# Optimization experiments

Measured on AMD Instinct MI355X. Metric: run time of the kernel, lower is better.

## Reference

```python
import jax, jax.numpy as jnp
import numpy as np
import math

B = 2
LAYERS = 18
LATENT = 512
MAPPER_LAYER = 7  # w_code_num[attention_layer=11]
CLUSTERS = 10
CLUSTER_LAYER = 11
CLUSTER_DIM = 512 + 2 * (512 // 16)  # 576
LR_MUL = 0.1
LAYER_NUM = [0, 2, 3, 5, 6, 8, 9, 11, 12, 14, 15, 17, 18, 20, 21, 23, 24]
CH = [512] * 11 + [256] * 2 + [128] * 3 + [64] * 3 + [32] * 3 + [16] * 3
RES = [4, 8, 8, 16, 16, 32, 32, 64, 64, 128, 128] + [256] * 14


def _forward(x, fmaps, mw, mb, afw, afb, aw, ab, alw, alb, initial_state):
    batch = x.shape[0]
    blend = fmaps[CLUSTER_LAYER - 1]
    size = blend.shape[2]  # 128

    # ---- cluster assignment (torch.no_grad block) ----
    pc = blend.shape[1] // 16  # position_channel = 32
    coords = jnp.arange(size, dtype=jnp.float32) * (2.0 / (size - 1)) - 1.0
    xp = jnp.broadcast_to(coords[None, :], (size, size))
    yp = jnp.broadcast_to(coords[:, None], (size, size))
    cf = jnp.concatenate([
        blend,
        jnp.broadcast_to(xp[None, None], (batch, pc, size, size)),
        jnp.broadcast_to(yp[None, None], (batch, pc, size, size)),
    ], axis=1)
    cf = jax.lax.stop_gradient(cf)
    flat = cf.transpose(0, 2, 3, 1).reshape(-1, cf.shape[1])  # [B*S*S, 576]
    dis = (jnp.sum(flat * flat, axis=1, keepdims=True)
           - 2.0 * flat @ initial_state.T
           + jnp.sum(initial_state * initial_state, axis=1)[None, :])
    assign = jnp.argmin(dis, axis=1).reshape(batch, size, size)
    choice = jnp.arange(batch)[:, None, None] * CLUSTERS + assign  # [B,S,S]

    x7 = x[:, :MAPPER_LAYER, -LATENT:]
    h = x7 * jax.lax.rsqrt(jnp.mean(x7 * x7, axis=-1, keepdims=True) + 1e-8)
    w_scale = (1.0 / math.sqrt(LATENT)) * LR_MUL
    for i in range(3):
        h = jnp.einsum('bci,coi->bco', h, mw[:, i]) * w_scale
        h = jax.nn.leaky_relu(h + mb[:, i][None] * LR_MUL, 0.2) * math.sqrt(2.0)
    delta_zs = jnp.concatenate(
        [h, jnp.zeros((batch, LAYERS - MAPPER_LAYER, LATENT), h.dtype)], axis=1)
    loss_delta = jnp.mean(jnp.sqrt(jnp.sum(delta_zs[:, :MAPPER_LAYER] ** 2, axis=-1)))

    # ---- attention branch (EqualConv2d 1x1 + nearest interpolate, torch semantics) ----
    def conv1x1(f, w, b):
        cin = f.shape[1]
        return jnp.einsum('bihw,oi->bohw', f, w) * (1.0 / math.sqrt(cin)) + b[None, :, None, None]

    def interp(f):  # torch nearest: src = floor(i * in / out)
        H = f.shape[2]
        idx = (jnp.arange(size) * H) // size
        return f[:, :, idx][:, :, :, idx]

    att = [interp(conv1x1(fmaps[-1], afw, afb))]
    for c in range(LAYERS - 1):
        f = fmaps[LAYER_NUM[c]]
        att.append(interp(conv1x1(f, aw[c][:, :f.shape[1]], ab[c])))
    amap = jnp.concatenate(att, axis=1)  # [B, 32*18, S, S]
    logits = jnp.einsum('bihw,i->bhw', amap, alw) * (1.0 / math.sqrt(32 * LAYERS)) + alb[0]
    each = jax.nn.sigmoid(logits)  # [B,S,S]

    # ---- training branch: per-(batch,cluster) masked mean -> segment mean ----
    nseg = batch * CLUSTERS
    seg = choice.reshape(-1)
    vals = each.reshape(-1)
    sums = jax.ops.segment_sum(vals, seg, num_segments=nseg)
    cnts = jax.ops.segment_sum(jnp.ones_like(vals), seg, num_segments=nseg)
    mean = sums / jnp.maximum(cnts, 1.0)
    attention_map = jnp.where(cnts > 0, mean, 1.0)[choice]  # [B,S,S]
    loss_reg = jnp.sum(jnp.where(cnts > 0, jnp.maximum(mean - 0.8, 0.0), 0.0)) / batch
    loss_tv = jnp.mean((each - jax.lax.stop_gradient(attention_map)) ** 2)

    am = attention_map[:, None]  # [B,1,S,S]
    final = jnp.where(am < 0.8, am - jax.lax.stop_gradient(am), am)
    # torchvision gaussian_blur(k=5): sigma = 0.3*((5-1)*0.5-1)+0.8 = 1.1, reflect pad
    xs = jnp.linspace(-2.0, 2.0, 5)
    k1 = jnp.exp(-0.5 * (xs / 1.1) ** 2)
    k1 = k1 / jnp.sum(k1)
    k2 = jnp.outer(k1, k1)[None, None]  # [1,1,5,5]
    padded = jnp.pad(final, ((0, 0), (0, 0), (2, 2), (2, 2)), mode='reflect')
    blurred = jax.lax.conv_general_dilated(padded, k2.astype(final.dtype), (1, 1), 'VALID')
    return delta_zs, blurred, loss_delta, loss_reg, loss_tv


def setup_inputs() -> dict:
    key = jax.random.key(0)
    ks = jax.random.split(key, 40)
    inp = {}
    inp['x'] = jax.random.normal(ks[0], (B, LAYERS, LATENT), jnp.float32)
    for i in range(25):
        inp[f'fmap_{i}'] = jax.random.normal(ks[1 + i], (B, CH[i], RES[i], RES[i]), jnp.float32)
    inp['fmap_25'] = jax.random.normal(ks[26], (B, 512, 4, 4), jnp.float32)
    inp['mw'] = jax.random.normal(ks[27], (MAPPER_LAYER, 3, LATENT, LATENT), jnp.float32)
    inp['mb'] = 0.1 * jax.random.normal(ks[28], (MAPPER_LAYER, 3, LATENT), jnp.float32)
    inp['afw'] = jax.random.normal(ks[29], (32, 512), jnp.float32)
    inp['afb'] = 0.1 * jax.random.normal(ks[30], (32,), jnp.float32)
    inp['aw'] = jax.random.normal(ks[31], (LAYERS - 1, 32, 512), jnp.float32)
    inp['ab'] = 0.1 * jax.random.normal(ks[32], (LAYERS - 1, 32), jnp.float32)
    inp['alw'] = jax.random.normal(ks[33], (32 * LAYERS,), jnp.float32)
    inp['alb'] = jnp.full((1,), 5.0, jnp.float32)  # attention_last bias init to 5
    inp['initial_state'] = jax.random.normal(ks[34], (CLUSTERS, CLUSTER_DIM), jnp.float32)
    inp['size'] = 128
    return inp


def reference(x, fmap_0, fmap_1, fmap_2, fmap_3, fmap_4, fmap_5, fmap_6, fmap_7,
              fmap_8, fmap_9, fmap_10, fmap_11, fmap_12, fmap_13, fmap_14, fmap_15,
              fmap_16, fmap_17, fmap_18, fmap_19, fmap_20, fmap_21, fmap_22, fmap_23,
              fmap_24, fmap_25, mw, mb, afw, afb, aw, ab, alw, alb, initial_state, size):
    fmaps = [fmap_0, fmap_1, fmap_2, fmap_3, fmap_4, fmap_5, fmap_6, fmap_7, fmap_8,
             fmap_9, fmap_10, fmap_11, fmap_12, fmap_13, fmap_14, fmap_15, fmap_16,
             fmap_17, fmap_18, fmap_19, fmap_20, fmap_21, fmap_22, fmap_23, fmap_24,
             fmap_25]
    return _forward(x, fmaps, mw, mb, afw, afb, aw, ab, alw, alb, initial_state)
```

## Files before the change

### kernel.cpp

```cpp
#include <hip/hip_runtime.h>
#include <math.h>

#define NPIX 32768
#define OUT_DZ 0
#define OUT_BLUR 18432
#define OUT_LD 51200
#define OUT_REG 51201
#define OUT_TV 51202
#define NSLAB 30

__constant__ int d_cin[18] = {512,512,512,512,512,512,512,512,256,256,128,128,64,64,32,32,16,16};
__constant__ int d_H[18]   = {4,  4,  8,  16, 32, 32, 64, 128,256,256,256,256,256,256,256,256,256,256};

__constant__ int d_slab_t[NSLAB]  = {0,1,2,3,4,5, 6,6, 7,7,7,7, 8,8,8,8, 9,9,9,9, 10,10, 11,11, 12,13,14,15,16,17};
__constant__ int d_slab_c0[NSLAB] = {0,0,0,0,0,0, 0,256, 0,128,256,384, 0,64,128,192, 0,64,128,192, 0,64, 0,64, 0,0,0,0,0,0};
__constant__ int d_slab_nc[NSLAB] = {512,512,512,512,512,512, 256,256, 128,128,128,128, 64,64,64,64, 64,64,64,64, 64,64, 64,64, 64,64,32,32,16,16};

struct FPtrs { const float* f[18]; };

#define WS_HA     0
#define WS_HB     7168
#define WS_ST     14336
#define WS_CN     22528
#define WS_BIASP  22576
#define WS_V      22656
#define WS_CHOICE 31872
#define WS_PART   64640
#define WS_EACH   1047680
#define WS_SUMS   1080448
#define WS_CNTS   1083008
#define WS_ATTV   1085568
#define WS_TVP    1085600

__global__ __launch_bounds__(512) void k_vfold(
    const float* __restrict__ afw, const float* __restrict__ afb,
    const float* __restrict__ aw,  const float* __restrict__ ab,
    const float* __restrict__ alw, const float* __restrict__ istate,
    float* __restrict__ v, float* __restrict__ biasp,
    float* __restrict__ st, float* __restrict__ cn)
{
    int t = blockIdx.x;
    if (t < 18) {
        int cin = d_cin[t];
        const float* w  = (t==0) ? afw : aw + (size_t)(t-1)*32*512;
        const float* bb = (t==0) ? afb : ab + (t-1)*32;
        float scale = (1.0f/sqrtf((float)cin)) * (1.0f/24.0f);
        int c = threadIdx.x;
        if (c < cin) {
            float s = 0.0f;
            #pragma unroll 8
            for (int o = 0; o < 32; o++) s += alw[t*32+o] * w[o*512 + c];
            v[t*512 + c] = s * scale;
        }
        if (threadIdx.x == 0) {
            float s = 0.0f;
            for (int o = 0; o < 32; o++) s += alw[t*32+o] * bb[o];
            biasp[t] = s * (1.0f/24.0f);
        }
    } else {
        int c = threadIdx.x;
        if (c < 512) {
            #pragma unroll
            for (int j = 0; j < 10; j++) st[c*16 + j] = -2.0f * istate[j*576 + c];
        }
        if (c < 10) {
            int j = c;
            float n = 0.0f, s1 = 0.0f, s2 = 0.0f;
            for (int k = 0; k < 576; k++) { float sv = istate[j*576+k]; n += sv*sv; }
            for (int k = 512; k < 544; k++) s1 += istate[j*576+k];
            for (int k = 544; k < 576; k++) s2 += istate[j*576+k];
            cn[j] = n; cn[16+j] = -2.0f*s1; cn[32+j] = -2.0f*s2;
        }
    }
}

__global__ __launch_bounds__(256) void k_assign(
    const float* __restrict__ blend, const float* __restrict__ st,
    const float* __restrict__ cn, int* __restrict__ choice)
{
    __shared__ float gsh[256*10];
    int tid = threadIdx.x;
    int csub = __builtin_amdgcn_readfirstlane(tid >> 6);
    int pl = tid & 63;
    int p = blockIdx.x*64 + pl;
    int b = p >> 14, rem = p & 16383;
    float g[10] = {0,0,0,0,0,0,0,0,0,0};
    const float* src = blend + ((size_t)b*512 + csub*128)*16384 + rem;
    const float* stc = st + csub*128*16;
    for (int c0 = 0; c0 < 128; c0 += 8) {
        float q[8];
        #pragma unroll
        for (int u = 0; u < 8; u++) q[u] = src[(size_t)(c0+u) << 14];
        #pragma unroll
        for (int u = 0; u < 8; u++) {
            #pragma unroll
            for (int j = 0; j < 10; j++) g[j] = fmaf(q[u], stc[(c0+u)*16 + j], g[j]);
        }
    }
    #pragma unroll
    for (int j = 0; j < 10; j++) gsh[tid*10 + j] = g[j];
    __syncthreads();
    if (tid < 64) {
        int pp = blockIdx.x*64 + tid;
        int bb = pp >> 14, rr = pp & 16383, y = rr >> 7, x = rr & 127;
        float cx = (float)x * (float)(2.0/127.0) - 1.0f;
        float cy = (float)y * (float)(2.0/127.0) - 1.0f;
        float gt[10];
        #pragma unroll
        for (int j = 0; j < 10; j++) {
            gt[j] = cn[j] + cn[16+j]*cx + cn[32+j]*cy
                  + gsh[tid*10 + j] + gsh[(64+tid)*10 + j]
                  + gsh[(128+tid)*10 + j] + gsh[(192+tid)*10 + j];
        }
        int best = 0; float bg = gt[0];
        #pragma unroll
        for (int j = 1; j < 10; j++) if (gt[j] < bg) { bg = gt[j]; best = j; }
        choice[pp] = bb*10 + best;
    }
}

__global__ __launch_bounds__(256) void k_norm(const float* __restrict__ x, float* __restrict__ h)
{
    int r = blockIdx.x;
    int b = r / 7, c = r % 7;
    const float* xr = x + ((size_t)b*18 + c)*512;
    int tid = threadIdx.x;
    float v0 = xr[tid], v1 = xr[tid+256];
    __shared__ float red[256];
    __shared__ float scale;
    red[tid] = v0*v0 + v1*v1; __syncthreads();
    for (int s = 128; s; s >>= 1) { if (tid < s) red[tid] += red[tid+s]; __syncthreads(); }
    if (tid == 0) scale = 1.0f / sqrtf(red[0]*(1.0f/512.0f) + 1e-8f);
    __syncthreads();
    h[r*512 + tid] = v0*scale; h[r*512 + 256 + tid] = v1*scale;
}

__global__ __launch_bounds__(256) void k_mlp(
    const float* __restrict__ mw, const float* __restrict__ mb,
    const float* __restrict__ hin, float* __restrict__ hout,
    int layer, float* __restrict__ dz)
{
    int wave = blockIdx.x*4 + (threadIdx.x >> 6);
    int lane = threadIdx.x & 63;
    int c = wave >> 9, o = wave & 511;
    const float* wrow = mw + (((size_t)(c*3 + layer)*512 + o) << 9) + lane*8;
    float4 w0 = *(const float4*)wrow;
    float4 w1 = *(const float4*)(wrow + 4);
    const float* h0 = hin + (size_t)c*512 + lane*8;
    const float* h1 = hin + (size_t)(7 + c)*512 + lane*8;
    float4 a0 = *(const float4*)h0, a1 = *(const float4*)(h0+4);
    float4 b0 = *(const float4*)h1, b1 = *(const float4*)(h1+4);
    float d0 = a0.x*w0.x + a0.y*w0.y + a0.z*w0.z + a0.w*w0.w
             + a1.x*w1.x + a1.y*w1.y + a1.z*w1.z + a1.w*w1.w;
    float d1 = b0.x*w0.x + b0.y*w0.y + b0.z*w0.z + b0.w*w0.w
             + b1.x*w1.x + b1.y*w1.y + b1.z*w1.z + b1.w*w1.w;
    #pragma unroll
    for (int m = 32; m; m >>= 1) { d0 += __shfl_xor(d0, m); d1 += __shfl_xor(d1, m); }
    if (lane == 0) {
        const float wsc = (float)(0.1/22.62741699796952);
        const float rt2 = 1.41421356237309515f;
        float bias = mb[(c*3 + layer)*512 + o] * 0.1f;
        float z0 = d0*wsc + bias; z0 = (z0 > 0.0f ? z0 : 0.2f*z0) * rt2;
        float z1 = d1*wsc + bias; z1 = (z1 > 0.0f ? z1 : 0.2f*z1) * rt2;
        hout[(size_t)c*512 + o] = z0;
        hout[(size_t)(7 + c)*512 + o] = z1;
        if (dz) {
            dz[((size_t)0*18 + c)*512 + o] = z0;
            dz[((size_t)1*18 + c)*512 + o] = z1;
        }
    }
}

__global__ __launch_bounds__(256) void k_lossdelta(const float* __restrict__ h, float* __restrict__ outp)
{
    __shared__ float red[256];
    int tid = threadIdx.x;
    float total = 0.0f;
    for (int r = 0; r < 14; r++) {
        float v0 = h[r*512 + tid], v1 = h[r*512 + 256 + tid];
        red[tid] = v0*v0 + v1*v1; __syncthreads();
        for (int s = 128; s; s >>= 1) { if (tid < s) red[tid] += red[tid+s]; __syncthreads(); }
        if (tid == 0) total += sqrtf(red[0]);
        __syncthreads();
    }
    if (tid == 0) outp[0] = total * (1.0f/14.0f);
}

__global__ __launch_bounds__(256) void k_zero(float* __restrict__ out)
{
    int z = blockIdx.x*256 + threadIdx.x;
    if (z < 11264) {
        int b = z / (11*512), rem = z % (11*512);
        out[(size_t)b*18*512 + 7*512 + rem] = 0.0f;
    }
}

__global__ __launch_bounds__(256) void k_each(FPtrs fp, const float* __restrict__ v, float* __restrict__ partial)
{
    __shared__ float vsh[512];
    int s  = blockIdx.x >> 6;
    int px = blockIdx.x & 63;
    int t  = d_slab_t[s];
    int c0 = d_slab_c0[s];
    int nc = d_slab_nc[s];
    int H  = d_H[t];
    int cin = d_cin[t];
    int tid  = threadIdx.x;
    for (int i = tid; i < nc; i += 256) vsh[i] = v[t*512 + c0 + i];
    __syncthreads();
    int row  = tid >> 6;
    int lane = tid & 63;
    int pbase = px*512;
    int b = pbase >> 14;
    int y = ((pbase & 16383) >> 7) + row;
    const float* base = fp.f[t] + (size_t)(b*cin + c0) * (size_t)(H*H);
    float a0 = 0.0f, a1 = 0.0f;

    if (H == 256) {
        const float* src = base + (size_t)(2*y)*256 + 4*lane;
        for (int cc = 0; cc < nc; cc += 8) {
            float4 q[8];
            #pragma unroll
            for (int u = 0; u < 8; u++) q[u] = *(const float4*)(src + (size_t)(cc+u)*65536);
            #pragma unroll
            for (int u = 0; u < 8; u++) {
                float vv = vsh[cc+u];
                a0 = fmaf(q[u].x, vv, a0); a1 = fmaf(q[u].z, vv, a1);
            }
        }
    } else if (H == 128) {
        const float* src = base + (size_t)y*128 + 2*lane;
        for (int cc = 0; cc < nc; cc += 8) {
            float2 q[8];
            #pragma unroll
            for (int u = 0; u < 8; u++) q[u] = *(const float2*)(src + (size_t)(cc+u)*16384);
            #pragma unroll
            for (int u = 0; u < 8; u++) {
                float vv = vsh[cc+u];
                a0 = fmaf(q[u].x, vv, a0); a1 = fmaf(q[u].y, vv, a1);
            }
        }
    } else if (H == 64) {
        const float* src = base + (size_t)(y >> 1)*64 + lane;
        for (int cc = 0; cc < nc; cc += 8) {
            float q[8];
            #pragma unroll
            for (int u = 0; u < 8; u++) q[u] = src[(size_t)(cc+u)*4096];
            #pragma unroll
            for (int u = 0; u < 8; u++) {
                float vv = vsh[cc+u];
                a0 = fmaf(q[u], vv, a0); a1 = fmaf(q[u], vv, a1);
            }
        }
    } else {
        int x0 = 2*lane, x1 = 2*lane + 1;
        int sy = (y*H) >> 7, sx0 = (x0*H) >> 7, sx1 = (x1*H) >> 7;
        const float* src = base + (size_t)sy*H;
        size_t HH = (size_t)H*H;
        for (int cc = 0; cc < nc; cc += 8) {
            float q0[8], q1[8];
            #pragma unroll
            for (int u = 0; u < 8; u++) {
                q0[u] = src[(size_t)(cc+u)*HH + sx0];
                q1[u] = src[(size_t)(cc+u)*HH + sx1];
            }
            #pragma unroll
            for (int u = 0; u < 8; u++) {
                float vv = vsh[cc+u];
                a0 = fmaf(q0[u], vv, a0); a1 = fmaf(q1[u], vv, a1);
            }
        }
    }
    int p = pbase + row*128 + 2*lane;
    float2 o; o.x = a0; o.y = a1;
    *(float2*)(partial + (size_t)s*NPIX + p) = o;
}

__global__ __launch_bounds__(256) void k_logits(
    const float* __restrict__ partial, const float* __restrict__ biasp,
    const float* __restrict__ alb, const int* __restrict__ choice,
    float* __restrict__ each, float* __restrict__ bsums, int* __restrict__ bcnts)
{
    __shared__ float ssum[20]; __shared__ int scnt[20]; __shared__ float sbias;
    int tid = threadIdx.x;
    if (tid < 20) { ssum[tid] = 0.0f; scnt[tid] = 0; }
    if (tid == 0) {
        float s = alb[0];
        for (int t = 0; t < 18; t++) s += biasp[t];
        sbias = s;
    }
    __syncthreads();
    int p = blockIdx.x*256 + tid;
    float lg = sbias;
    #pragma unroll
    for (int s = 0; s < NSLAB; s++) lg += partial[(size_t)s*NPIX + p];
    float e = 1.0f / (1.0f + expf(-lg));
    each[p] = e;
    int ch = choice[p];
    atomicAdd(&ssum[ch], e);
    atomicAdd(&scnt[ch], 1);
    __syncthreads();
    if (tid < 20) { bsums[blockIdx.x*20 + tid] = ssum[tid]; bcnts[blockIdx.x*20 + tid] = scnt[tid]; }
}

__global__ __launch_bounds__(64) void k_stats(
    const float* __restrict__ bsums, const int* __restrict__ bcnts,
    float* __restrict__ attv, float* __restrict__ out)
{
    __shared__ float red[32];
    int j = threadIdx.x;
    float regj = 0.0f;
    if (j < 20) {
        float s = 0.0f; int c = 0;
        for (int blk = 0; blk < 128; blk++) { s += bsums[blk*20 + j]; c += bcnts[blk*20 + j]; }
        float mean = s / fmaxf((float)c, 1.0f);
        attv[j] = (c > 0) ? mean : 1.0f;
        regj = (c > 0) ? fmaxf(mean - 0.8f, 0.0f) : 0.0f;
    }
    if (j < 32) red[j] = (j < 20) ? regj : 0.0f;
    __syncthreads();
    for (int s = 16; s; s >>= 1) { if (j < s) red[j] += red[j+s]; __syncthreads(); }
    if (j == 0) out[OUT_REG] = red[0] * 0.5f;
}

__global__ __launch_bounds__(256) void k_final(
    const float* __restrict__ each, const int* __restrict__ choice,
    const float* __restrict__ attv, float* __restrict__ tvp, float* __restrict__ out)
{
    __shared__ float av[20];
    __shared__ float red[256];
    int tid = threadIdx.x;
    if (tid < 20) av[tid] = attv[tid];
    __syncthreads();
    int p = blockIdx.x*256 + tid;
    int b = p >> 14, rem = p & 16383, y = rem >> 7, x = rem & 127;
    float k1[5]; float ks = 0.0f;
    #pragma unroll
    for (int i = 0; i < 5; i++) { float d = (float)(i-2) / 1.1f; k1[i] = expf(-0.5f*d*d); ks += k1[i]; }
    #pragma unroll
    for (int i = 0; i < 5; i++) k1[i] /= ks;
    const int* cb = choice + b*16384;
    float acc = 0.0f;
    #pragma unroll
    for (int a = 0; a < 5; a++) {
        int yy = y + a - 2; yy = (yy < 0) ? -yy : ((yy > 127) ? 254 - yy : yy);
        #pragma unroll
        for (int bb = 0; bb < 5; bb++) {
            int xx = x + bb - 2; xx = (xx < 0) ? -xx : ((xx > 127) ? 254 - xx : xx);
            float am = av[cb[yy*128 + xx]];
            float fin = (am < 0.8f) ? 0.0f : am;
            acc += k1[a]*k1[bb]*fin;
        }
    }
    out[OUT_BLUR + p] = acc;
    float amc = av[cb[y*128 + x]];
    float d = each[p] - amc;
    red[tid] = d*d; __syncthreads();
    for (int s = 128; s; s >>= 1) { if (tid < s) red[tid] += red[tid+s]; __syncthreads(); }
    if (tid == 0) tvp[blockIdx.x] = red[0];
}

__global__ __launch_bounds__(128) void k_tvred(const float* __restrict__ tvp, float* __restrict__ out)
{
    __shared__ float red[128];
    int tid = threadIdx.x;
    red[tid] = tvp[tid]; __syncthreads();
    for (int s = 64; s; s >>= 1) { if (tid < s) red[tid] += red[tid+s]; __syncthreads(); }
    if (tid == 0) out[OUT_TV] = red[0] * (1.0f/32768.0f);
}

extern "C" void kernel_launch(void* const* d_in, const int* in_sizes, int n_in,
                              void* d_out, int out_size, void* d_ws, size_t ws_size,
                              hipStream_t stream)
{
    const float* x      = (const float*)d_in[0];
    const float* blend  = (const float*)d_in[11];
    const float* mw     = (const float*)d_in[27];
    const float* mb     = (const float*)d_in[28];
    const float* afw    = (const float*)d_in[29];
    const float* afb    = (const float*)d_in[30];
    const float* aw     = (const float*)d_in[31];
    const float* ab     = (const float*)d_in[32];
    const float* alw    = (const float*)d_in[33];
    const float* alb    = (const float*)d_in[34];
    const float* istate = (const float*)d_in[35];
    float* out = (float*)d_out;
    float* ws  = (float*)d_ws;

    static const int LN[17] = {0,2,3,5,6,8,9,11,12,14,15,17,18,20,21,23,24};
    FPtrs fp;
    fp.f[0] = (const float*)d_in[26];
    for (int c = 0; c < 17; c++) fp.f[1+c] = (const float*)d_in[1 + LN[c]];

    float* hA     = ws + WS_HA;
    float* hB     = ws + WS_HB;
    float* st     = ws + WS_ST;
    float* cn     = ws + WS_CN;
    float* biasp  = ws + WS_BIASP;
    float* v      = ws + WS_V;
    int*   choice = (int*)(ws + WS_CHOICE);
    float* part   = ws + WS_PART;
    float* each   = ws + WS_EACH;
    float* bsums  = ws + WS_SUMS;
    int*   bcnts  = (int*)(ws + WS_CNTS);
    float* attv   = ws + WS_ATTV;
    float* tvp    = ws + WS_TVP;

    k_vfold<<<dim3(19), 512, 0, stream>>>(afw, afb, aw, ab, alw, istate, v, biasp, st, cn);
    k_norm<<<14, 256, 0, stream>>>(x, hA);
    k_mlp<<<896, 256, 0, stream>>>(mw, mb, hA, hB, 0, nullptr);
    k_mlp<<<896, 256, 0, stream>>>(mw, mb, hB, hA, 1, nullptr);
    k_mlp<<<896, 256, 0, stream>>>(mw, mb, hA, hB, 2, out + OUT_DZ);
    k_lossdelta<<<1, 256, 0, stream>>>(hB, out + OUT_LD);
    k_zero<<<44, 256, 0, stream>>>(out);
    k_assign<<<512, 256, 0, stream>>>(blend, st, cn, choice);
    k_each<<<NSLAB*64, 256, 0, stream>>>(fp, v, part);
    k_logits<<<128, 256, 0, stream>>>(part, biasp, alb, choice, each, bsums, bcnts);
    k_stats<<<1, 64, 0, stream>>>(bsums, bcnts, attv, out);
    k_final<<<128, 256, 0, stream>>>(each, choice, attv, tvp, out);
    k_tvred<<<1, 128, 0, stream>>>(tvp, out);
}
```

Measured before the change: 159.7 us.

## Retile attention partial sums and cluster assignment for more pixels per thread

Splits the large-resolution feature maps into finer channel slabs (48 instead of 30) and gives those slabs a new block mapping where each wave handles four rows with wider float4 loads. Cluster assignment now uses 512-thread blocks where each thread covers two pixels and each of eight waves sums 64 channels. The aim is more memory-level parallelism and better occupancy on the bandwidth-bound feature-map reads. In exchange, more partial-sum slabs must be written and reduced in the logits kernel, and the workspace offsets grow to fit them.

After: 163.5 us. 1.02x slower.

```diff
diff --git a/kernel.cpp b/kernel.cpp
--- a/kernel.cpp
+++ b/kernel.cpp
@@ -7,14 +7,29 @@
 #define OUT_LD 51200
 #define OUT_REG 51201
 #define OUT_TV 51202
-#define NSLAB 30
+#define NSLAB 48
 
 __constant__ int d_cin[18] = {512,512,512,512,512,512,512,512,256,256,128,128,64,64,32,32,16,16};
 __constant__ int d_H[18]   = {4,  4,  8,  16, 32, 32, 64, 128,256,256,256,256,256,256,256,256,256,256};
 
-__constant__ int d_slab_t[NSLAB]  = {0,1,2,3,4,5, 6,6, 7,7,7,7, 8,8,8,8, 9,9,9,9, 10,10, 11,11, 12,13,14,15,16,17};
-__constant__ int d_slab_c0[NSLAB] = {0,0,0,0,0,0, 0,256, 0,128,256,384, 0,64,128,192, 0,64,128,192, 0,64, 0,64, 0,0,0,0,0,0};
-__constant__ int d_slab_nc[NSLAB] = {512,512,512,512,512,512, 256,256, 128,128,128,128, 64,64,64,64, 64,64,64,64, 64,64, 64,64, 64,64,32,32,16,16};
+__constant__ int d_slab_t[NSLAB]  = {0,1,2,3,4,5, 6,6,
+                                     7,7,7,7,7,7,7,7,
+                                     8,8,8,8,8,8,8,8,
+                                     9,9,9,9,9,9,9,9,
+                                     10,10,10,10, 11,11,11,11,
+                                     12,12, 13,13, 14, 15, 16, 17};
+__constant__ int d_slab_c0[NSLAB] = {0,0,0,0,0,0, 0,256,
+                                     0,64,128,192,256,320,384,448,
+                                     0,32,64,96,128,160,192,224,
+                                     0,32,64,96,128,160,192,224,
+                                     0,32,64,96, 0,32,64,96,
+                                     0,32, 0,32, 0, 0, 0, 0};
+__constant__ int d_slab_nc[NSLAB] = {512,512,512,512,512,512, 256,256,
+                                     64,64,64,64,64,64,64,64,
+                                     32,32,32,32,32,32,32,32,
+                                     32,32,32,32,32,32,32,32,
+                                     32,32,32,32, 32,32,32,32,
+                                     32,32, 32,32, 32, 32, 16, 16};
 
 struct FPtrs { const float* f[18]; };
 
@@ -26,11 +41,11 @@
 #define WS_V      22656
 #define WS_CHOICE 31872
 #define WS_PART   64640
-#define WS_EACH   1047680
-#define WS_SUMS   1080448
-#define WS_CNTS   1083008
-#define WS_ATTV   1085568
-#define WS_TVP    1085600
+#define WS_EACH   1637504
+#define WS_SUMS   1670272
+#define WS_CNTS   1672832
+#define WS_ATTV   1675392
+#define WS_TVP    1675424
 
 __global__ __launch_bounds__(512) void k_vfold(
     const float* __restrict__ afw, const float* __restrict__ afb,
@@ -74,48 +89,57 @@
     }
 }
 
-__global__ __launch_bounds__(256) void k_assign(
+__global__ __launch_bounds__(512, 4) void k_assign(
     const float* __restrict__ blend, const float* __restrict__ st,
     const float* __restrict__ cn, int* __restrict__ choice)
 {
-    __shared__ float gsh[256*10];
-    int tid = threadIdx.x;
-    int csub = __builtin_amdgcn_readfirstlane(tid >> 6);
-    int pl = tid & 63;
-    int p = blockIdx.x*64 + pl;
-    int b = p >> 14, rem = p & 16383;
-    float g[10] = {0,0,0,0,0,0,0,0,0,0};
-    const float* src = blend + ((size_t)b*512 + csub*128)*16384 + rem;
-    const float* stc = st + csub*128*16;
-    for (int c0 = 0; c0 < 128; c0 += 8) {
-        float q[8];
+    __shared__ float gsh[8*128*10];
+    int tid = threadIdx.x;
+    int w = tid >> 6, lane = tid & 63;
+    int csub = __builtin_amdgcn_readfirstlane(w);
+    int pw = blockIdx.x * 128;
+    int b = pw >> 14, rem = pw & 16383;
+    const float* src = blend + ((size_t)b*512 + csub*64)*16384 + rem + 2*lane;
+    const float* stc = st + csub*64*16;
+    float g0[10] = {0,0,0,0,0,0,0,0,0,0};
+    float g1[10] = {0,0,0,0,0,0,0,0,0,0};
+    for (int c0 = 0; c0 < 64; c0 += 4) {
+        float2 q[4];
         #pragma unroll
-        for (int u = 0; u < 8; u++) q[u] = src[(size_t)(c0+u) << 14];
+        for (int u = 0; u < 4; u++) q[u] = *(const float2*)(src + (size_t)(c0+u)*16384);
         #pragma unroll
-        for (int u = 0; u < 8; u++) {
-            #pragma unroll
-            for (int j = 0; j < 10; j++) g[j] = fmaf(q[u], stc[(c0+u)*16 + j], g[j]);
+        for (int u = 0; u < 4; u++) {
+            #pragma unroll
+            for (int j = 0; j < 10; j++) {
+                float sv = stc[(c0+u)*16 + j];
+                g0[j] = fmaf(q[u].x, sv, g0[j]);
+                g1[j] = fmaf(q[u].y, sv, g1[j]);
+            }
         }
     }
     #pragma unroll
-    for (int j = 0; j < 10; j++) gsh[tid*10 + j] = g[j];
-    __syncthreads();
-    if (tid < 64) {
-        int pp = blockIdx.x*64 + tid;
-        int bb = pp >> 14, rr = pp & 16383, y = rr >> 7, x = rr & 127;
+    for (int j = 0; j < 10; j++) {
+        gsh[(w*128 + 2*lane)*10 + j]     = g0[j];
+        gsh[(w*128 + 2*lane + 1)*10 + j] = g1[j];
+    }
+    __syncthreads();
+    if (tid < 128) {
+        int p = pw + tid;
+        int bb = p >> 14, rr = p & 16383, y = rr >> 7, x = rr & 127;
         float cx = (float)x * (float)(2.0/127.0) - 1.0f;
         float cy = (float)y * (float)(2.0/127.0) - 1.0f;
         float gt[10];
         #pragma unroll
         for (int j = 0; j < 10; j++) {
-            gt[j] = cn[j] + cn[16+j]*cx + cn[32+j]*cy
-                  + gsh[tid*10 + j] + gsh[(64+tid)*10 + j]
-                  + gsh[(128+tid)*10 + j] + gsh[(192+tid)*10 + j];
+            float acc = cn[j] + cn[16+j]*cx + cn[32+j]*cy;
+            #pragma unroll
+            for (int ww = 0; ww < 8; ww++) acc += gsh[(ww*128 + tid)*10 + j];
+            gt[j] = acc;
         }
         int best = 0; float bg = gt[0];
         #pragma unroll
         for (int j = 1; j < 10; j++) if (gt[j] < bg) { bg = gt[j]; best = j; }
-        choice[pp] = bb*10 + best;
+        choice[p] = bb*10 + best;
     }
 }
 
@@ -195,52 +219,90 @@
     }
 }
 
-__global__ __launch_bounds__(256) void k_each(FPtrs fp, const float* __restrict__ v, float* __restrict__ partial)
+__global__ __launch_bounds__(256, 4) void k_each(FPtrs fp, const float* __restrict__ v, float* __restrict__ partial)
 {
     __shared__ float vsh[512];
-    int s  = blockIdx.x >> 6;
-    int px = blockIdx.x & 63;
+    int bid = blockIdx.x;
+    int tid = threadIdx.x;
+    int s = (bid < 512) ? (bid >> 6) : (8 + ((bid - 512) >> 4));
     int t  = d_slab_t[s];
     int c0 = d_slab_c0[s];
     int nc = d_slab_nc[s];
     int H  = d_H[t];
     int cin = d_cin[t];
-    int tid  = threadIdx.x;
     for (int i = tid; i < nc; i += 256) vsh[i] = v[t*512 + c0 + i];
     __syncthreads();
-    int row  = tid >> 6;
-    int lane = tid & 63;
-    int pbase = px*512;
+    int w = tid >> 6, lane = tid & 63;
+
+    if (bid >= 512) {
+        int sub = (bid - 512) & 15;
+        int b = sub >> 3, rowgrp = sub & 7;
+        int y0 = rowgrp*16 + w*4;
+        const float* base = fp.f[t] + (size_t)(b*cin + c0) * (size_t)H * (size_t)H;
+        float* pout = partial + (size_t)s*NPIX + b*16384;
+        if (H == 256) {
+            float a[4][2] = {{0,0},{0,0},{0,0},{0,0}};
+            const float* srcr[4];
+            #pragma unroll
+            for (int i = 0; i < 4; i++) srcr[i] = base + (size_t)(2*(y0+i))*256 + 4*lane;
+            for (int cc = 0; cc < nc; cc += 2) {
+                float4 q[2][4];
+                #pragma unroll
+                for (int u = 0; u < 2; u++)
+                    #pragma unroll
+                    for (int i = 0; i < 4; i++)
+                        q[u][i] = *(const float4*)(srcr[i] + (size_t)(cc+u)*65536);
+                #pragma unroll
+                for (int u = 0; u < 2; u++) {
+                    float vv = vsh[cc+u];
+                    #pragma unroll
+                    for (int i = 0; i < 4; i++) {
+                        a[i][0] = fmaf(q[u][i].x, vv, a[i][0]);
+                        a[i][1] = fmaf(q[u][i].z, vv, a[i][1]);
+                    }
+                }
+            }
+            #pragma unroll
+            for (int i = 0; i < 4; i++) {
+                float2 o; o.x = a[i][0]; o.y = a[i][1];
+                *(float2*)(pout + (y0+i)*128 + 2*lane) = o;
+            }
+        } else {
+            int h = lane >> 5, c4 = 4*(lane & 31);
+            float aA[4] = {0,0,0,0}, aB[4] = {0,0,0,0};
+            const float* srcA = base + (size_t)(y0 + h)*128 + c4;
+            const float* srcB = base + (size_t)(y0 + 2 + h)*128 + c4;
+            for (int cc = 0; cc < nc; cc += 4) {
+                float4 qa[4], qb[4];
+                #pragma unroll
+                for (int u = 0; u < 4; u++) {
+                    qa[u] = *(const float4*)(srcA + (size_t)(cc+u)*16384);
+                    qb[u] = *(const float4*)(srcB + (size_t)(cc+u)*16384);
+                }
+                #pragma unroll
+                for (int u = 0; u < 4; u++) {
+                    float vv = vsh[cc+u];
+                    aA[0] = fmaf(qa[u].x, vv, aA[0]); aA[1] = fmaf(qa[u].y, vv, aA[1]);
+                    aA[2] = fmaf(qa[u].z, vv, aA[2]); aA[3] = fmaf(qa[u].w, vv, aA[3]);
+                    aB[0] = fmaf(qb[u].x, vv, aB[0]); aB[1] = fmaf(qb[u].y, vv, aB[1]);
+                    aB[2] = fmaf(qb[u].z, vv, aB[2]); aB[3] = fmaf(qb[u].w, vv, aB[3]);
+                }
+            }
+            float4 oA; oA.x=aA[0]; oA.y=aA[1]; oA.z=aA[2]; oA.w=aA[3];
+            float4 oB; oB.x=aB[0]; oB.y=aB[1]; oB.z=aB[2]; oB.w=aB[3];
+            *(float4*)(pout + (y0+h)*128 + c4) = oA;
+            *(float4*)(pout + (y0+2+h)*128 + c4) = oB;
+        }
+        return;
+    }
+
+    int px = bid & 63;
+    int row = w, pbase = px*512;
     int b = pbase >> 14;
     int y = ((pbase & 16383) >> 7) + row;
     const float* base = fp.f[t] + (size_t)(b*cin + c0) * (size_t)(H*H);
     float a0 = 0.0f, a1 = 0.0f;
-
-    if (H == 256) {
-        const float* src = base + (size_t)(2*y)*256 + 4*lane;
-        for (int cc = 0; cc < nc; cc += 8) {
-            float4 q[8];
-            #pragma unroll
-            for (int u = 0; u < 8; u++) q[u] = *(const float4*)(src + (size_t)(cc+u)*65536);
-            #pragma unroll
-            for (int u = 0; u < 8; u++) {
-                float vv = vsh[cc+u];
-                a0 = fmaf(q[u].x, vv, a0); a1 = fmaf(q[u].z, vv, a1);
-            }
-        }
-    } else if (H == 128) {
-        const float* src = base + (size_t)y*128 + 2*lane;
-        for (int cc = 0; cc < nc; cc += 8) {
-            float2 q[8];
-            #pragma unroll
-            for (int u = 0; u < 8; u++) q[u] = *(const float2*)(src + (size_t)(cc+u)*16384);
-            #pragma unroll
-            for (int u = 0; u < 8; u++) {
-                float vv = vsh[cc+u];
-                a0 = fmaf(q[u].x, vv, a0); a1 = fmaf(q[u].y, vv, a1);
-            }
-        }
-    } else if (H == 64) {
+    if (H == 64) {
         const float* src = base + (size_t)(y >> 1)*64 + lane;
         for (int cc = 0; cc < nc; cc += 8) {
             float q[8];
@@ -292,7 +354,7 @@
     __syncthreads();
     int p = blockIdx.x*256 + tid;
     float lg = sbias;
-    #pragma unroll
+    #pragma unroll 8
     for (int s = 0; s < NSLAB; s++) lg += partial[(size_t)s*NPIX + p];
     float e = 1.0f / (1.0f + expf(-lg));
     each[p] = e;
@@ -413,8 +475,8 @@
     k_mlp<<<896, 256, 0, stream>>>(mw, mb, hA, hB, 2, out + OUT_DZ);
     k_lossdelta<<<1, 256, 0, stream>>>(hB, out + OUT_LD);
     k_zero<<<44, 256, 0, stream>>>(out);
-    k_assign<<<512, 256, 0, stream>>>(blend, st, cn, choice);
-    k_each<<<NSLAB*64, 256, 0, stream>>>(fp, v, part);
+    k_assign<<<256, 512, 0, stream>>>(blend, st, cn, choice);
+    k_each<<<512 + (NSLAB-8)*16, 256, 0, stream>>>(fp, v, part);
     k_logits<<<128, 256, 0, stream>>>(part, biasp, alb, choice, each, bsums, bcnts);
     k_stats<<<1, 64, 0, stream>>>(bsums, bcnts, attv, out);
     k_final<<<128, 256, 0, stream>>>(each, choice, attv, tvp, out);
```

## Double-buffer high-resolution layer loads via async global-to-LDS copies

Applied to the files above, without the earlier changes.

Splits the per-pixel attention reduction into two kernels. A heavy kernel covers the 128/256-resolution layers, one block per layer and pixel tile, and streams 8-channel chunks into double-buffered LDS using global_load_lds so the next loads overlap the current FMAs. A light kernel keeps the old direct-load path for the small layers. Dropping the channel-slab split shrinks the partial-sum buffer from 30 to 18 slabs, which cuts the logits reads. The cost is fewer, longer blocks, 64KB of LDS per block that limits occupancy, and two barriers per phase.

Measured after the change: 194.9 us. 22.1% more time.

```diff
diff --git a/kernel.cpp b/kernel.cpp
--- a/kernel.cpp
+++ b/kernel.cpp
@@ -7,14 +7,9 @@
 #define OUT_LD 51200
 #define OUT_REG 51201
 #define OUT_TV 51202
-#define NSLAB 30
 
 __constant__ int d_cin[18] = {512,512,512,512,512,512,512,512,256,256,128,128,64,64,32,32,16,16};
 __constant__ int d_H[18]   = {4,  4,  8,  16, 32, 32, 64, 128,256,256,256,256,256,256,256,256,256,256};
-
-__constant__ int d_slab_t[NSLAB]  = {0,1,2,3,4,5, 6,6, 7,7,7,7, 8,8,8,8, 9,9,9,9, 10,10, 11,11, 12,13,14,15,16,17};
-__constant__ int d_slab_c0[NSLAB] = {0,0,0,0,0,0, 0,256, 0,128,256,384, 0,64,128,192, 0,64,128,192, 0,64, 0,64, 0,0,0,0,0,0};
-__constant__ int d_slab_nc[NSLAB] = {512,512,512,512,512,512, 256,256, 128,128,128,128, 64,64,64,64, 64,64,64,64, 64,64, 64,64, 64,64,32,32,16,16};
 
 struct FPtrs { const float* f[18]; };
 
@@ -26,11 +21,11 @@
 #define WS_V      22656
 #define WS_CHOICE 31872
 #define WS_PART   64640
-#define WS_EACH   1047680
-#define WS_SUMS   1080448
-#define WS_CNTS   1083008
-#define WS_ATTV   1085568
-#define WS_TVP    1085600
+#define WS_EACH   654464
+#define WS_SUMS   687232
+#define WS_CNTS   689792
+#define WS_ATTV   692352
+#define WS_TVP    692384
 
 __global__ __launch_bounds__(512) void k_vfold(
     const float* __restrict__ afw, const float* __restrict__ afb,
@@ -195,52 +190,113 @@
     }
 }
 
-__global__ __launch_bounds__(256) void k_each(FPtrs fp, const float* __restrict__ v, float* __restrict__ partial)
-{
+__global__ __launch_bounds__(256) void k_heavy(FPtrs fp, const float* __restrict__ v, float* __restrict__ partial)
+{
+    __shared__ float buf[2][8192];
     __shared__ float vsh[512];
-    int s  = blockIdx.x >> 6;
-    int px = blockIdx.x & 63;
-    int t  = d_slab_t[s];
-    int c0 = d_slab_c0[s];
-    int nc = d_slab_nc[s];
+    int bid = blockIdx.x;
+    int t  = 7 + (bid >> 6);
+    int sub = bid & 63;
+    int b  = sub >> 5;
+    int rb = sub & 31;
+    int ch = d_cin[t];
     int H  = d_H[t];
-    int cin = d_cin[t];
-    int tid  = threadIdx.x;
-    for (int i = tid; i < nc; i += 256) vsh[i] = v[t*512 + c0 + i];
-    __syncthreads();
-    int row  = tid >> 6;
-    int lane = tid & 63;
+    int tid = threadIdx.x;
+    int w = tid >> 6, lane = tid & 63;
+    const float* base = fp.f[t] + (size_t)b*ch*(size_t)H*H;
+    for (int i = tid; i < ch; i += 256) vsh[i] = v[t*512 + i];
+
+    int NP = ch >> 3;
+    if (H == 256) {
+        #pragma unroll
+        for (int k = 0; k < 2; k++) {
+            int cp = 2*w + k;
+            const float* src = base + (size_t)cp*65536 + (size_t)(8*rb)*256 + lane*4;
+            #pragma unroll
+            for (int i = 0; i < 4; i++)
+                __builtin_amdgcn_global_load_lds(src + i*512, &buf[0][cp*1024 + i*256], 16, 0, 0);
+        }
+    } else {
+        #pragma unroll
+        for (int k = 0; k < 2; k++) {
+            int cp = 2*w + k;
+            const float* srcb = base + (size_t)cp*16384 + (size_t)(4*rb)*128;
+            #pragma unroll
+            for (int j = 0; j < 2; j++)
+                __builtin_amdgcn_global_load_lds(srcb + (2*j + (lane>>5))*128 + (lane&31)*4,
+                                                 &buf[0][cp*1024 + j*256], 16, 0, 0);
+        }
+    }
+
+    float2 acc; acc.x = 0.0f; acc.y = 0.0f;
+    for (int ph = 0; ph < NP; ph++) {
+        int pb = ph & 1;
+        if (ph + 1 < NP) {
+            int nb = pb ^ 1;
+            int cbase = (ph + 1) << 3;
+            if (H == 256) {
+                #pragma unroll
+                for (int k = 0; k < 2; k++) {
+                    int cp = 2*w + k;
+                    const float* src = base + (size_t)(cbase + cp)*65536 + (size_t)(8*rb)*256 + lane*4;
+                    #pragma unroll
+                    for (int i = 0; i < 4; i++)
+                        __builtin_amdgcn_global_load_lds(src + i*512, &buf[nb][cp*1024 + i*256], 16, 0, 0);
+                }
+            } else {
+                #pragma unroll
+                for (int k = 0; k < 2; k++) {
+                    int cp = 2*w + k;
+                    const float* srcb = base + (size_t)(cbase + cp)*16384 + (size_t)(4*rb)*128;
+                    #pragma unroll
+                    for (int j = 0; j < 2; j++)
+                        __builtin_amdgcn_global_load_lds(srcb + (2*j + (lane>>5))*128 + (lane&31)*4,
+                                                         &buf[nb][cp*1024 + j*256], 16, 0, 0);
+                }
+            }
+        }
+        __syncthreads();
+        int cb = ph << 3;
+        if (H == 256) {
+            #pragma unroll
+            for (int cp = 0; cp < 8; cp++) {
+                float4 q = *(const float4*)&buf[pb][cp*1024 + w*256 + lane*4];
+                float vv = vsh[cb + cp];
+                acc.x = fmaf(q.x, vv, acc.x);
+                acc.y = fmaf(q.z, vv, acc.y);
+            }
+        } else {
+            #pragma unroll
+            for (int cp = 0; cp < 8; cp++) {
+                float2 q = *(const float2*)&buf[pb][cp*1024 + w*128 + lane*2];
+                float vv = vsh[cb + cp];
+                acc.x = fmaf(q.x, vv, acc.x);
+                acc.y = fmaf(q.y, vv, acc.y);
+            }
+        }
+        __syncthreads();
+    }
+    *(float2*)(partial + (size_t)t*NPIX + b*16384 + (rb*4 + w)*128 + 2*lane) = acc;
+}
+
+__global__ __launch_bounds__(256) void k_light(FPtrs fp, const float* __restrict__ v, float* __restrict__ partial)
+{
+    __shared__ float vsh[512];
+    int bid = blockIdx.x;
+    int tid = threadIdx.x;
+    int t  = bid >> 6;
+    int nc = d_cin[t];
+    int H  = d_H[t];
+    for (int i = tid; i < nc; i += 256) vsh[i] = v[t*512 + i];
+    __syncthreads();
+    int w = tid >> 6, lane = tid & 63;
+    int px = bid & 63;
     int pbase = px*512;
     int b = pbase >> 14;
-    int y = ((pbase & 16383) >> 7) + row;
-    const float* base = fp.f[t] + (size_t)(b*cin + c0) * (size_t)(H*H);
+    int y = ((pbase & 16383) >> 7) + w;
+    const float* base = fp.f[t] + (size_t)b*nc*(size_t)(H*H);
     float a0 = 0.0f, a1 = 0.0f;
-
-    if (H == 256) {
-        const float* src = base + (size_t)(2*y)*256 + 4*lane;
-        for (int cc = 0; cc < nc; cc += 8) {
-            float4 q[8];
-            #pragma unroll
-            for (int u = 0; u < 8; u++) q[u] = *(const float4*)(src + (size_t)(cc+u)*65536);
-            #pragma unroll
-            for (int u = 0; u < 8; u++) {
-                float vv = vsh[cc+u];
-                a0 = fmaf(q[u].x, vv, a0); a1 = fmaf(q[u].z, vv, a1);
-            }
-        }
-    } else if (H == 128) {
-        const float* src = base + (size_t)y*128 + 2*lane;
-        for (int cc = 0; cc < nc; cc += 8) {
-            float2 q[8];
-            #pragma unroll
-            for (int u = 0; u < 8; u++) q[u] = *(const float2*)(src + (size_t)(cc+u)*16384);
-            #pragma unroll
-            for (int u = 0; u < 8; u++) {
-                float vv = vsh[cc+u];
-                a0 = fmaf(q[u].x, vv, a0); a1 = fmaf(q[u].y, vv, a1);
-            }
-        }
-    } else if (H == 64) {
+    if (H == 64) {
         const float* src = base + (size_t)(y >> 1)*64 + lane;
         for (int cc = 0; cc < nc; cc += 8) {
             float q[8];
@@ -271,9 +327,9 @@
             }
         }
     }
-    int p = pbase + row*128 + 2*lane;
+    int p = pbase + w*128 + 2*lane;
     float2 o; o.x = a0; o.y = a1;
-    *(float2*)(partial + (size_t)s*NPIX + p) = o;
+    *(float2*)(partial + (size_t)t*NPIX + p) = o;
 }
 
 __global__ __launch_bounds__(256) void k_logits(
@@ -293,7 +349,7 @@
     int p = blockIdx.x*256 + tid;
     float lg = sbias;
     #pragma unroll
-    for (int s = 0; s < NSLAB; s++) lg += partial[(size_t)s*NPIX + p];
+    for (int s = 0; s < 18; s++) lg += partial[(size_t)s*NPIX + p];
     float e = 1.0f / (1.0f + expf(-lg));
     each[p] = e;
     int ch = choice[p];
@@ -414,7 +470,8 @@
     k_lossdelta<<<1, 256, 0, stream>>>(hB, out + OUT_LD);
     k_zero<<<44, 256, 0, stream>>>(out);
     k_assign<<<512, 256, 0, stream>>>(blend, st, cn, choice);
-    k_each<<<NSLAB*64, 256, 0, stream>>>(fp, v, part);
+    k_heavy<<<11*64, 256, 0, stream>>>(fp, v, part);
+    k_light<<<7*64, 256, 0, stream>>>(fp, v, part);
     k_logits<<<128, 256, 0, stream>>>(part, biasp, alb, choice, each, bsums, bcnts);
     k_stats<<<1, 64, 0, stream>>>(bsums, bcnts, attv, out);
     k_final<<<128, 256, 0, stream>>>(each, choice, attv, tvp, out);
```
